# Performance work log

Measured on AMD Instinct MI355X. Metric: run time of the kernel, lower is better.

The kernel has to match this reference:

```python
import jax, jax.numpy as jnp
import numpy as np

ES = 256
NUM_SPECIES, NUM_ABILITIES, NUM_ITEMS, NUM_MOVES = 1026, 300, 500, 920
NUM_ITEM_EFFECTS, NUM_GENDERS, NUM_STATUS, NUM_VOLATILE_STATUS = 16, 3, 8, 105
B, N, F = 8192, 12, 42
# feature layout (flat int32 vector per entity)
(SPECIES, ABILITY, ITEM, ITEM_EFFECT, GENDER, STATUS, BEING_CALLED_BACK, TRAPPED,
 NEWLY_SWITCHED, TOXIC_TURNS, SLEEP_TURNS, FAINTED, ACTIVE, SIDE, LEVEL, HP, MAXHP) = range(17)
BOOST0, VOL0, MOVEID0, MOVEPP0 = 17, 24, 33, 37  # 7 boosts, 9 volatile words, 4 moves, 4 pp

DENSE_DIMS = [("hp", 10), ("level", 7), ("active", 2), ("onehot", 32), ("boosts", 7),
              ("volatiles", NUM_VOLATILE_STATUS), ("item", ES + NUM_ITEM_EFFECTS),
              ("side", 2), ("moves", ES + 6)]

def _bits(x, world_dim):
    # binary-scale embedding: bit decomposition of an int feature
    nb = (world_dim - 1).bit_length()
    mask = jnp.asarray(1 << np.arange(nb), dtype=jnp.int32)
    return ((x[..., None] & mask) != 0).astype(jnp.float32)

def setup_inputs() -> dict:
    key = jax.random.key(0)
    ks = jax.random.split(key, 32)
    s = 0.02
    inp = {"entities": jax.random.randint(ks[0], (B, N, F), 0, 2, dtype=jnp.int32)}
    inp["embed_species"] = jax.random.normal(ks[1], (NUM_SPECIES, ES), jnp.float32) * s
    inp["embed_ability"] = jax.random.normal(ks[2], (NUM_ABILITIES, ES), jnp.float32) * s
    inp["embed_item"] = jax.random.normal(ks[3], (NUM_ITEMS, ES), jnp.float32) * s
    inp["embed_moves"] = jax.random.normal(ks[4], (NUM_MOVES, ES), jnp.float32) * s
    for i, (name, din) in enumerate(DENSE_DIMS):
        inp[f"{name}_W"] = jax.random.normal(ks[5 + i], (din, ES), jnp.float32) * s
        inp[f"{name}_b"] = jnp.zeros((ES,), jnp.float32)
    return inp

def _forward(entities, embed_species, embed_ability, embed_item, embed_moves,
             hp_W, hp_b, level_W, level_b, active_W, active_b, onehot_W, onehot_b,
             boosts_W, boosts_b, volatiles_W, volatiles_b, item_W, item_b,
             side_W, side_b, moves_W, moves_b):
    e = entities
    oh = jax.nn.one_hot
    dense = lambda x, W, b: x @ W + b
    hp = e[..., HP].astype(jnp.float32)
    maxhp = jnp.clip(e[..., MAXHP], 1).astype(jnp.float32)
    hp_ratio = jnp.clip(hp / maxhp, 0.0, 1.0)                      # (B,N)
    hp_token = jnp.floor(1023.0 * hp_ratio).astype(jnp.int32)
    boolean_code = jnp.concatenate([
        hp_ratio[..., None], oh(e[..., GENDER], NUM_GENDERS), oh(e[..., STATUS], NUM_STATUS),
        oh(e[..., BEING_CALLED_BACK], 2), oh(e[..., TRAPPED], 2), oh(e[..., NEWLY_SWITCHED], 2),
        oh(e[..., TOXIC_TURNS], 8), oh(e[..., SLEEP_TURNS], 4), oh(e[..., FAINTED], 2)], axis=-1)  # (B,N,32)
    item_onehot = jnp.concatenate([embed_item[e[..., ITEM]], oh(e[..., ITEM_EFFECT], NUM_ITEM_EFFECTS)], axis=-1)
    boosts = e[..., BOOST0:VOL0].astype(jnp.float32) / 2.0          # (B,N,7)
    vol = e[..., VOL0:VOL0 + 9]
    vbits = (vol[..., None] & jnp.arange(16)) > 0                   # (B,N,9,16)
    vol_oh = vbits.reshape(*vol.shape[:-1], 144)[..., :NUM_VOLATILE_STATUS].astype(jnp.float32)
    moveset = jnp.concatenate([embed_moves[e[..., MOVEID0:MOVEPP0]],
                               _bits(e[..., MOVEPP0:MOVEPP0 + 4], 64)], axis=-1)  # (B,N,4,262)
    moves_out = jnp.einsum('bnmf,fd->bnd', moveset, moves_W) + 4.0 * moves_b      # sum of 4 Dense outputs
    emb = (dense(_bits(hp_token, 1024), hp_W, hp_b)
           + dense(_bits(e[..., LEVEL], 101), level_W, level_b)
           + dense(oh(e[..., ACTIVE], 2), active_W, active_b)
           + dense(boolean_code, onehot_W, onehot_b)
           + dense(boosts, boosts_W, boosts_b)
           + dense(vol_oh, volatiles_W, volatiles_b)
           + embed_species[e[..., SPECIES]]
           + embed_ability[e[..., ABILITY]]
           + dense(item_onehot, item_W, item_b)
           + dense(oh(e[..., SIDE], 2), side_W, side_b)
           + moves_out)
    return emb

def reference(entities, embed_species, embed_ability, embed_item, embed_moves,
              hp_W, hp_b, level_W, level_b, active_W, active_b, onehot_W, onehot_b,
              boosts_W, boosts_b, volatiles_W, volatiles_b, item_W, item_b,
              side_W, side_b, moves_W, moves_b):
    return _forward(entities, embed_species, embed_ability, embed_item, embed_moves,
                    hp_W, hp_b, level_W, level_b, active_W, active_b, onehot_W, onehot_b,
                    boosts_W, boosts_b, volatiles_W, volatiles_b, item_W, item_b,
                    side_W, side_b, moves_W, moves_b)
```

## Files before the change

kernel.cpp:

```cpp
#include <hip/hip_runtime.h>
#include <hip/hip_fp16.h>

#define ES 256
#define NFEAT 42
#define NENT (8192 * 12)

#define F_SPECIES 0
#define F_ABILITY 1
#define F_ITEM 2
#define F_ITEM_EFFECT 3
#define F_GENDER 4
#define F_STATUS 5
#define F_BCB 6
#define F_TRAPPED 7
#define F_NEWSW 8
#define F_TOXIC 9
#define F_SLEEP 10
#define F_FAINTED 11
#define F_ACTIVE 12
#define F_SIDE 13
#define F_LEVEL 14
#define F_HP 15
#define F_MAXHP 16
#define F_BOOST0 17
#define F_VOL0 24
#define F_MOVEID0 33
#define F_MOVEPP0 37

#define OFF_HP     0
#define OFF_LV     (OFF_HP + 1024*ES)
#define OFF_PP     (OFF_LV + 128*ES)
#define OFF_VP     (OFF_PP + 64*ES)
#define OFF_CA     (OFF_VP + 784*ES)
#define OFF_CB     (OFF_CA + 768*ES)
#define OFF_EI     (OFF_CB + 1024*ES)
#define OFF_EM     (OFF_EI + 500*ES)
#define OFF_SP     (OFF_EM + 920*ES)
#define OFF_AB     (OFF_SP + 1026*ES)
#define WS_HALVES  (OFF_AB + 300*ES)

typedef float vf4 __attribute__((ext_vector_type(4)));

__device__ __forceinline__ float4 ld4(const float* p) {
    return *reinterpret_cast<const float4*>(p);
}
__device__ __forceinline__ void st4(float* p, const float4 v) {
    *reinterpret_cast<float4*>(p) = v;
}
__device__ __forceinline__ void st4_nt(float* p, const float4 v) {
    vf4 t = {v.x, v.y, v.z, v.w};
    __builtin_nontemporal_store(t, reinterpret_cast<vf4*>(p));
}
__device__ __forceinline__ void add4(float4& a, const float4 b) {
    a.x += b.x; a.y += b.y; a.z += b.z; a.w += b.w;
}
__device__ __forceinline__ float4 sum4(const float4 a, const float4 b) {
    return make_float4(a.x + b.x, a.y + b.y, a.z + b.z, a.w + b.w);
}
__device__ __forceinline__ void fma4(float4& a, float s, const float4 b) {
    a.x += s * b.x; a.y += s * b.y; a.z += s * b.z; a.w += s * b.w;
}
__device__ __forceinline__ int sclamp(int x, int lo, int hi) {
    return x < lo ? lo : (x > hi ? hi : x);
}
__device__ __forceinline__ void st4h(__half* p, const float4 v) {
    __half2 a = __floats2half2_rn(v.x, v.y);
    __half2 b = __floats2half2_rn(v.z, v.w);
    uint2 u;
    u.x = *reinterpret_cast<unsigned*>(&a);
    u.y = *reinterpret_cast<unsigned*>(&b);
    *reinterpret_cast<uint2*>(p) = u;
}

#define TB_HP0 0
#define TB_LV0 256
#define TB_PP0 288
#define TB_VP0 304
#define TB_CA0 500
#define TB_CB0 692
#define TB_EI0 948
#define TB_EM0 1073
#define TB_SP0 1303
#define TB_AB0 1560
#define TB_TOT 1635

__global__ __launch_bounds__(256) void k_tables(
    const float* __restrict__ sp_e, const float* __restrict__ ab_e,
    const float* __restrict__ item_e, const float* __restrict__ moves_e,
    const float* __restrict__ hp_W, const float* __restrict__ level_W,
    const float* __restrict__ moves_W, const float* __restrict__ vol_W,
    const float* __restrict__ item_W, const float* __restrict__ onehot_W,
    const float* __restrict__ active_W, const float* __restrict__ side_W,
    const float* __restrict__ hp_b, const float* __restrict__ level_b,
    const float* __restrict__ active_b, const float* __restrict__ onehot_b,
    const float* __restrict__ boosts_b, const float* __restrict__ vol_b,
    const float* __restrict__ item_b, const float* __restrict__ side_b,
    const float* __restrict__ moves_b,
    __half* __restrict__ wh) {
    __shared__ float4 se4[4][64];
    const int bid = blockIdx.x, tid = threadIdx.x;
    const int rl = tid >> 6, lane = tid & 63, d0 = lane * 4;
    float4 acc = make_float4(0.f, 0.f, 0.f, 0.f);

    if (bid < TB_LV0) {
        int v = (bid - TB_HP0) * 4 + rl;
        for (int b = 0; b < 10; ++b)
            if ((v >> b) & 1) add4(acc, ld4(hp_W + b * ES + d0));
        st4h(wh + OFF_HP + v * ES + d0, acc);
    } else if (bid < TB_PP0) {
        int v = (bid - TB_LV0) * 4 + rl;
        for (int b = 0; b < 7; ++b)
            if ((v >> b) & 1) add4(acc, ld4(level_W + b * ES + d0));
        st4h(wh + OFF_LV + v * ES + d0, acc);
    } else if (bid < TB_VP0) {
        int v = (bid - TB_PP0) * 4 + rl;
        for (int b = 0; b < 6; ++b)
            if ((v >> b) & 1) add4(acc, ld4(moves_W + (256 + b) * ES + d0));
        st4h(wh + OFF_PP + v * ES + d0, acc);
    } else if (bid < TB_CA0) {
        int v = (bid - TB_VP0) * 4 + rl;
        if (v < 768) {
            int t = v >> 8, pair = v & 255, a = pair >> 4, b = pair & 15;
            for (int j = 0; j < 16; ++j) {
                if (a & j) add4(acc, ld4(vol_W + (32 * t + j) * ES + d0));
                if (b & j) add4(acc, ld4(vol_W + (32 * t + 16 + j) * ES + d0));
            }
        } else {
            int a = v - 768;
            for (int j = 0; j < 9; ++j)
                if (a & j) add4(acc, ld4(vol_W + (96 + j) * ES + d0));
        }
        st4h(wh + OFF_VP + v * ES + d0, acc);
    } else if (bid < TB_CB0) {
        int idx = (bid - TB_CA0) * 4 + rl;
        int fa = idx & 1, ns = (idx >> 1) & 1, tr = (idx >> 2) & 1, bcb = (idx >> 3) & 1;
        int rest = idx >> 4, g = rest % 3, e = rest / 3;
        acc = sum4(sum4(ld4(item_W + (256 + e) * ES + d0), ld4(onehot_W + (1 + g) * ES + d0)),
                   sum4(ld4(onehot_W + (12 + bcb) * ES + d0), ld4(onehot_W + (14 + tr) * ES + d0)));
        add4(acc, sum4(ld4(onehot_W + (16 + ns) * ES + d0), ld4(onehot_W + (30 + fa) * ES + d0)));
        st4h(wh + OFF_CA + idx * ES + d0, acc);
    } else if (bid < TB_EI0) {
        int idx = (bid - TB_CB0) * 4 + rl;
        int sd = idx & 1, act = (idx >> 1) & 1, sl = (idx >> 2) & 3,
            tox = (idx >> 4) & 7, st = idx >> 7;
        acc = sum4(sum4(ld4(hp_b + d0), ld4(level_b + d0)),
                   sum4(ld4(active_b + d0), ld4(onehot_b + d0)));
        add4(acc, sum4(ld4(boosts_b + d0), ld4(vol_b + d0)));
        add4(acc, sum4(ld4(item_b + d0), ld4(side_b + d0)));
        fma4(acc, 4.0f, ld4(moves_b + d0));
        add4(acc, sum4(ld4(onehot_W + (4 + st) * ES + d0), ld4(onehot_W + (18 + tox) * ES + d0)));
        add4(acc, sum4(ld4(onehot_W + (26 + sl) * ES + d0),
                       sum4(ld4(active_W + act * ES + d0), ld4(side_W + sd * ES + d0))));
        st4h(wh + OFF_CB + idx * ES + d0, acc);
    } else if (bid < TB_SP0) {
        const float* E; const float* W; __half* o; int r0;
        if (bid < TB_EM0) { E = item_e;  W = item_W;  o = wh + OFF_EI; r0 = (bid - TB_EI0) * 4; }
        else              { E = moves_e; W = moves_W; o = wh + OFF_EM; r0 = (bid - TB_EM0) * 4; }
        se4[tid >> 6][tid & 63] = ld4(E + r0 * ES + tid * 4);
        __syncthreads();
#pragma unroll 4
        for (int k0 = 0; k0 < 64; ++k0) {
            float4 e4 = se4[rl][k0];
            fma4(acc, e4.x, ld4(W + (4 * k0 + 0) * ES + d0));
            fma4(acc, e4.y, ld4(W + (4 * k0 + 1) * ES + d0));
            fma4(acc, e4.z, ld4(W + (4 * k0 + 2) * ES + d0));
            fma4(acc, e4.w, ld4(W + (4 * k0 + 3) * ES + d0));
        }
        st4h(o + (r0 + rl) * ES + d0, acc);
    } else if (bid < TB_AB0) {
        int r = (bid - TB_SP0) * 4 + rl;
        if (r < 1026) st4h(wh + OFF_SP + r * ES + d0, ld4(sp_e + r * ES + d0));
    } else {
        int r = (bid - TB_AB0) * 4 + rl;
        st4h(wh + OFF_AB + r * ES + d0, ld4(ab_e + r * ES + d0));
    }
}


__global__ __launch_bounds__(256) void k_main(
    const int* __restrict__ ent,
    const float* __restrict__ onehotW, const float* __restrict__ boostsW,
    const __half* __restrict__ wh,
    float* __restrict__ out) {
    __shared__ float lds[8 * ES];
    {
        int t = threadIdx.x;
        int row = t >> 5, col = (t & 31) * 8;
        const float* src = (row < 7) ? (boostsW + row * ES + col) : (onehotW + col);
        st4(&lds[row * ES + col], ld4(src));
        st4(&lds[row * ES + col + 4], ld4(src + 4));
    }
    __syncthreads();

    const int lane  = threadIdx.x & 63;
    const int wpair = __builtin_amdgcn_readfirstlane((blockIdx.x * 256 + threadIdx.x) >> 6);
    const int entA  = wpair * 2;
    const int e     = lane >> 5;
    const int sub   = lane & 31;
    const int sub8  = sub * 8;
    const int base  = entA * NFEAT;

    const int fv  = __builtin_nontemporal_load(ent + base + lane);
    const int fv2 = __builtin_nontemporal_load(ent + base + 52 + sub);

#define RLA(i) __builtin_amdgcn_readlane(fv, (i))
#define RLB(i) ((i) < 22 ? __builtin_amdgcn_readlane(fv, 42 + (i)) \
                         : __builtin_amdgcn_readlane(fv2, (i) - 10))

    const __half* Hp = wh + OFF_HP;
    const __half* Lv = wh + OFF_LV;
    const __half* Pp = wh + OFF_PP;
    const __half* VP = wh + OFF_VP;
    const __half* CA = wh + OFF_CA;
    const __half* CB = wh + OFF_CB;
    const __half* EI = wh + OFF_EI;
    const __half* EM = wh + OFF_EM;
    const __half* SP = wh + OFF_SP;
    const __half* AB = wh + OFF_AB;

#define IDX_BLOCK(RL, S) \
    const int iCB##S = ((((RL(F_STATUS) & 7) * 8 + (RL(F_TOXIC) & 7)) * 4 + (RL(F_SLEEP) & 3)) * 2 + \
                        (RL(F_ACTIVE) & 1)) * 2 + (RL(F_SIDE) & 1); \
    const int iCA##S = (((((RL(F_ITEM_EFFECT) & 15) * 3 + sclamp(RL(F_GENDER), 0, 2)) * 2 + \
                          (RL(F_BCB) & 1)) * 2 + (RL(F_TRAPPED) & 1)) * 2 + \
                        (RL(F_NEWSW) & 1)) * 2 + (RL(F_FAINTED) & 1); \
    const int iSP##S = sclamp(RL(F_SPECIES), 0, 1025); \
    const int iAB##S = sclamp(RL(F_ABILITY), 0, 299); \
    const int iIT##S = sclamp(RL(F_ITEM), 0, 499); \
    float hpv##S = (float)RL(F_HP); \
    int mh##S = RL(F_MAXHP); if (mh##S < 1) mh##S = 1; \
    const float ratio##S = fminf(fmaxf(hpv##S / (float)mh##S, 0.f), 1.f); \
    const int tok##S = (int)floorf(1023.f * ratio##S); \
    const int iLV##S = RL(F_LEVEL) & 127; \
    const int vp0##S = ((RL(F_VOL0 + 0) & 15) << 4) | (RL(F_VOL0 + 1) & 15); \
    const int vp1##S = ((RL(F_VOL0 + 2) & 15) << 4) | (RL(F_VOL0 + 3) & 15); \
    const int vp2##S = ((RL(F_VOL0 + 4) & 15) << 4) | (RL(F_VOL0 + 5) & 15); \
    const int v6##S  = RL(F_VOL0 + 6) & 15; \
    const int m0##S = sclamp(RL(F_MOVEID0 + 0), 0, 919), m1##S = sclamp(RL(F_MOVEID0 + 1), 0, 919), \
              m2##S = sclamp(RL(F_MOVEID0 + 2), 0, 919), m3##S = sclamp(RL(F_MOVEID0 + 3), 0, 919); \
    const int p0##S = RL(F_MOVEPP0 + 0) & 63, p1##S = RL(F_MOVEPP0 + 1) & 63, \
              p2##S = RL(F_MOVEPP0 + 2) & 63, p3##S = RL(F_MOVEPP0 + 3) & 63; \
    const float b0##S = (float)RL(F_BOOST0 + 0), b1##S = (float)RL(F_BOOST0 + 1), \
                b2##S = (float)RL(F_BOOST0 + 2), b3##S = (float)RL(F_BOOST0 + 3), \
                b4##S = (float)RL(F_BOOST0 + 4), b5##S = (float)RL(F_BOOST0 + 5), \
                b6##S = (float)RL(F_BOOST0 + 6);

    IDX_BLOCK(RLA, A)
    IDX_BLOCK(RLB, B)
#undef RLA
#undef RLB
#undef IDX_BLOCK

#define SEL(x) (e ? x##B : x##A)
    const int jCB = SEL(iCB), jCA = SEL(iCA), jSP = SEL(iSP), jAB = SEL(iAB), jIT = SEL(iIT);
    const int jHP = SEL(tok), jLV = SEL(iLV);
    const int jV0 = SEL(vp0), jV1 = SEL(vp1), jV2 = SEL(vp2), jV6 = SEL(v6);
    const int jP0 = SEL(p0), jP1 = SEL(p1), jP2 = SEL(p2), jP3 = SEL(p3);
    const int jM0 = SEL(m0), jM1 = SEL(m1), jM2 = SEL(m2), jM3 = SEL(m3);
    const float ratio = SEL(ratio);
    const float s0v = 0.5f * SEL(b0), s1v = 0.5f * SEL(b1), s2v = 0.5f * SEL(b2),
                s3v = 0.5f * SEL(b3), s4v = 0.5f * SEL(b4), s5v = 0.5f * SEL(b5),
                s6v = 0.5f * SEL(b6);
#undef SEL

#define LD8(n, tab, idx) const uint4 n = *reinterpret_cast<const uint4*>((tab) + (idx) * ES + sub8)
    LD8(uCB, CB, jCB);
    LD8(uCA, CA, jCA);
    LD8(uSP, SP, jSP);
    LD8(uAB, AB, jAB);
    LD8(uIT, EI, jIT);
    LD8(uHP, Hp, jHP);
    LD8(uLV, Lv, jLV);
    LD8(uV0, VP, 0 * 256 + jV0);
    LD8(uV1, VP, 1 * 256 + jV1);
    LD8(uV2, VP, 2 * 256 + jV2);
    LD8(uV6, VP, 768 + jV6);
    LD8(uP0, Pp, jP0);
    LD8(uP1, Pp, jP1);
    LD8(uP2, Pp, jP2);
    LD8(uP3, Pp, jP3);
    LD8(uE0, EM, jM0);
    LD8(uE1, EM, jM1);
    LD8(uE2, EM, jM2);
    LD8(uE3, EM, jM3);
#undef LD8

    float4 a0 = make_float4(0.f, 0.f, 0.f, 0.f);
    float4 a1 = make_float4(0.f, 0.f, 0.f, 0.f);
#define ACC(u) { \
    __half2 h; float2 f; \
    h = *reinterpret_cast<const __half2*>(&u.x); f = __half22float2(h); a0.x += f.x; a0.y += f.y; \
    h = *reinterpret_cast<const __half2*>(&u.y); f = __half22float2(h); a0.z += f.x; a0.w += f.y; \
    h = *reinterpret_cast<const __half2*>(&u.z); f = __half22float2(h); a1.x += f.x; a1.y += f.y; \
    h = *reinterpret_cast<const __half2*>(&u.w); f = __half22float2(h); a1.z += f.x; a1.w += f.y; }
    ACC(uCB) ACC(uCA) ACC(uSP) ACC(uAB) ACC(uIT) ACC(uHP) ACC(uLV)
    ACC(uV0) ACC(uV1) ACC(uV2) ACC(uV6)
    ACC(uP0) ACC(uP1) ACC(uP2) ACC(uP3)
    ACC(uE0) ACC(uE1) ACC(uE2) ACC(uE3)
#undef ACC

    fma4(a0, ratio, ld4(&lds[7 * ES + sub8]));     fma4(a1, ratio, ld4(&lds[7 * ES + sub8 + 4]));
    fma4(a0, s0v, ld4(&lds[0 * ES + sub8]));       fma4(a1, s0v, ld4(&lds[0 * ES + sub8 + 4]));
    fma4(a0, s1v, ld4(&lds[1 * ES + sub8]));       fma4(a1, s1v, ld4(&lds[1 * ES + sub8 + 4]));
    fma4(a0, s2v, ld4(&lds[2 * ES + sub8]));       fma4(a1, s2v, ld4(&lds[2 * ES + sub8 + 4]));
    fma4(a0, s3v, ld4(&lds[3 * ES + sub8]));       fma4(a1, s3v, ld4(&lds[3 * ES + sub8 + 4]));
    fma4(a0, s4v, ld4(&lds[4 * ES + sub8]));       fma4(a1, s4v, ld4(&lds[4 * ES + sub8 + 4]));
    fma4(a0, s5v, ld4(&lds[5 * ES + sub8]));       fma4(a1, s5v, ld4(&lds[5 * ES + sub8 + 4]));
    fma4(a0, s6v, ld4(&lds[6 * ES + sub8]));       fma4(a1, s6v, ld4(&lds[6 * ES + sub8 + 4]));

    float* op = out + (entA + e) * ES + sub8;
    st4_nt(op, a0);
    st4_nt(op + 4, a1);
}


extern "C" void kernel_launch(void* const* d_in, const int* in_sizes, int n_in,
                              void* d_out, int out_size, void* d_ws, size_t ws_size,
                              hipStream_t stream) {
    const int*   entities = (const int*)  d_in[0];
    const float* sp       = (const float*)d_in[1];
    const float* ab       = (const float*)d_in[2];
    const float* item_e   = (const float*)d_in[3];
    const float* moves_e  = (const float*)d_in[4];
    const float* hp_W     = (const float*)d_in[5];
    const float* hp_b     = (const float*)d_in[6];
    const float* level_W  = (const float*)d_in[7];
    const float* level_b  = (const float*)d_in[8];
    const float* active_W = (const float*)d_in[9];
    const float* active_b = (const float*)d_in[10];
    const float* onehot_W = (const float*)d_in[11];
    const float* onehot_b = (const float*)d_in[12];
    const float* boosts_W = (const float*)d_in[13];
    const float* boosts_b = (const float*)d_in[14];
    const float* vol_W    = (const float*)d_in[15];
    const float* vol_b    = (const float*)d_in[16];
    const float* item_W   = (const float*)d_in[17];
    const float* item_b   = (const float*)d_in[18];
    const float* side_W   = (const float*)d_in[19];
    const float* side_b   = (const float*)d_in[20];
    const float* moves_W  = (const float*)d_in[21];
    const float* moves_b  = (const float*)d_in[22];

    __half* wh  = (__half*)d_ws;
    float*  out = (float*)d_out;

    k_tables<<<TB_TOT, 256, 0, stream>>>(
        sp, ab, item_e, moves_e, hp_W, level_W, moves_W, vol_W,
        item_W, onehot_W, active_W, side_W,
        hp_b, level_b, active_b, onehot_b, boosts_b,
        vol_b, item_b, side_b, moves_b, wh);

    k_main<<<NENT / 8, 256, 0, stream>>>(entities, onehot_W, boosts_W, wh, out);
}
```

Measured before the change: 212.0 us.

## Precompute boost-pair and hp-ratio contributions into fp16 lookup tables

Folds the hp ratio term into the hp token table and builds new fp16 tables for boost pairs (13x13) and the last boost. The main kernel no longer stages boosts and onehot weights in LDS or runs a block barrier, and replaces the FMAs with four extra gathers. It also precomputes byte offsets per lookup. The cost is more gather traffic per entity, and the ratio term is now quantized to the hp token with fp16 rounding. Boost values are also clamped to the range -6 to 6.

New measurement: 214.0 us. Within noise of the previous version (+0.9%).

```diff
diff --git a/kernel.cpp b/kernel.cpp
--- a/kernel.cpp
+++ b/kernel.cpp
@@ -37,15 +37,16 @@
 #define OFF_EM     (OFF_EI + 500*ES)
 #define OFF_SP     (OFF_EM + 920*ES)
 #define OFF_AB     (OFF_SP + 1026*ES)
-#define WS_HALVES  (OFF_AB + 300*ES)
+#define OFF_B01    (OFF_AB + 300*ES)
+#define OFF_B23    (OFF_B01 + 169*ES)
+#define OFF_B45    (OFF_B23 + 169*ES)
+#define OFF_B6     (OFF_B45 + 169*ES)
+#define WS_HALVES  (OFF_B6 + 13*ES)
 
 typedef float vf4 __attribute__((ext_vector_type(4)));
 
 __device__ __forceinline__ float4 ld4(const float* p) {
     return *reinterpret_cast<const float4*>(p);
-}
-__device__ __forceinline__ void st4(float* p, const float4 v) {
-    *reinterpret_cast<float4*>(p) = v;
 }
 __device__ __forceinline__ void st4_nt(float* p, const float4 v) {
     vf4 t = {v.x, v.y, v.z, v.w};
@@ -82,7 +83,8 @@
 #define TB_EM0 1073
 #define TB_SP0 1303
 #define TB_AB0 1560
-#define TB_TOT 1635
+#define TB_BP0 1635
+#define TB_TOT 1765
 
 __global__ __launch_bounds__(256) void k_tables(
     const float* __restrict__ sp_e, const float* __restrict__ ab_e,
@@ -91,6 +93,7 @@
     const float* __restrict__ moves_W, const float* __restrict__ vol_W,
     const float* __restrict__ item_W, const float* __restrict__ onehot_W,
     const float* __restrict__ active_W, const float* __restrict__ side_W,
+    const float* __restrict__ boosts_W,
     const float* __restrict__ hp_b, const float* __restrict__ level_b,
     const float* __restrict__ active_b, const float* __restrict__ onehot_b,
     const float* __restrict__ boosts_b, const float* __restrict__ vol_b,
@@ -106,6 +109,7 @@
         int v = (bid - TB_HP0) * 4 + rl;
         for (int b = 0; b < 10; ++b)
             if ((v >> b) & 1) add4(acc, ld4(hp_W + b * ES + d0));
+        fma4(acc, (float)v * (1.0f / 1023.0f), ld4(onehot_W + d0));
         st4h(wh + OFF_HP + v * ES + d0, acc);
     } else if (bid < TB_PP0) {
         int v = (bid - TB_LV0) * 4 + rl;
@@ -170,34 +174,37 @@
     } else if (bid < TB_AB0) {
         int r = (bid - TB_SP0) * 4 + rl;
         if (r < 1026) st4h(wh + OFF_SP + r * ES + d0, ld4(sp_e + r * ES + d0));
-    } else {
+    } else if (bid < TB_BP0) {
         int r = (bid - TB_AB0) * 4 + rl;
         st4h(wh + OFF_AB + r * ES + d0, ld4(ab_e + r * ES + d0));
+    } else {
+        int r = (bid - TB_BP0) * 4 + rl;
+        if (r < 507) {
+            int pair = r / 169;
+            int rr = r - pair * 169;
+            int i = rr / 13, j = rr % 13;
+            fma4(acc, 0.5f * (float)(i - 6), ld4(boosts_W + (2 * pair) * ES + d0));
+            fma4(acc, 0.5f * (float)(j - 6), ld4(boosts_W + (2 * pair + 1) * ES + d0));
+            st4h(wh + OFF_B01 + r * ES + d0, acc);
+        } else {
+            int b = r - 507;
+            fma4(acc, 0.5f * (float)(b - 6), ld4(boosts_W + 6 * ES + d0));
+            st4h(wh + OFF_B6 + b * ES + d0, acc);
+        }
     }
 }
 
 
 __global__ __launch_bounds__(256) void k_main(
     const int* __restrict__ ent,
-    const float* __restrict__ onehotW, const float* __restrict__ boostsW,
     const __half* __restrict__ wh,
     float* __restrict__ out) {
-    __shared__ float lds[8 * ES];
-    {
-        int t = threadIdx.x;
-        int row = t >> 5, col = (t & 31) * 8;
-        const float* src = (row < 7) ? (boostsW + row * ES + col) : (onehotW + col);
-        st4(&lds[row * ES + col], ld4(src));
-        st4(&lds[row * ES + col + 4], ld4(src + 4));
-    }
-    __syncthreads();
-
     const int lane  = threadIdx.x & 63;
     const int wpair = __builtin_amdgcn_readfirstlane((blockIdx.x * 256 + threadIdx.x) >> 6);
     const int entA  = wpair * 2;
     const int e     = lane >> 5;
     const int sub   = lane & 31;
-    const int sub8  = sub * 8;
+    const int sub16 = sub * 16;
     const int base  = entA * NFEAT;
 
     const int fv  = __builtin_nontemporal_load(ent + base + lane);
@@ -207,108 +214,89 @@
 #define RLB(i) ((i) < 22 ? __builtin_amdgcn_readlane(fv, 42 + (i)) \
                          : __builtin_amdgcn_readlane(fv2, (i) - 10))
 
-    const __half* Hp = wh + OFF_HP;
-    const __half* Lv = wh + OFF_LV;
-    const __half* Pp = wh + OFF_PP;
-    const __half* VP = wh + OFF_VP;
-    const __half* CA = wh + OFF_CA;
-    const __half* CB = wh + OFF_CB;
-    const __half* EI = wh + OFF_EI;
-    const __half* EM = wh + OFF_EM;
-    const __half* SP = wh + OFF_SP;
-    const __half* AB = wh + OFF_AB;
-
+#define GOFF(OFF, idx) (((OFF) * 2) + ((idx) << 9))
 #define IDX_BLOCK(RL, S) \
-    const int iCB##S = ((((RL(F_STATUS) & 7) * 8 + (RL(F_TOXIC) & 7)) * 4 + (RL(F_SLEEP) & 3)) * 2 + \
-                        (RL(F_ACTIVE) & 1)) * 2 + (RL(F_SIDE) & 1); \
-    const int iCA##S = (((((RL(F_ITEM_EFFECT) & 15) * 3 + sclamp(RL(F_GENDER), 0, 2)) * 2 + \
+    const int oCB##S = GOFF(OFF_CB, ((((RL(F_STATUS) & 7) * 8 + (RL(F_TOXIC) & 7)) * 4 + (RL(F_SLEEP) & 3)) * 2 + \
+                        (RL(F_ACTIVE) & 1)) * 2 + (RL(F_SIDE) & 1)); \
+    const int oCA##S = GOFF(OFF_CA, (((((RL(F_ITEM_EFFECT) & 15) * 3 + sclamp(RL(F_GENDER), 0, 2)) * 2 + \
                           (RL(F_BCB) & 1)) * 2 + (RL(F_TRAPPED) & 1)) * 2 + \
-                        (RL(F_NEWSW) & 1)) * 2 + (RL(F_FAINTED) & 1); \
-    const int iSP##S = sclamp(RL(F_SPECIES), 0, 1025); \
-    const int iAB##S = sclamp(RL(F_ABILITY), 0, 299); \
-    const int iIT##S = sclamp(RL(F_ITEM), 0, 499); \
+                        (RL(F_NEWSW) & 1)) * 2 + (RL(F_FAINTED) & 1)); \
+    const int oSP##S = GOFF(OFF_SP, sclamp(RL(F_SPECIES), 0, 1025)); \
+    const int oAB##S = GOFF(OFF_AB, sclamp(RL(F_ABILITY), 0, 299)); \
+    const int oIT##S = GOFF(OFF_EI, sclamp(RL(F_ITEM), 0, 499)); \
     float hpv##S = (float)RL(F_HP); \
     int mh##S = RL(F_MAXHP); if (mh##S < 1) mh##S = 1; \
     const float ratio##S = fminf(fmaxf(hpv##S / (float)mh##S, 0.f), 1.f); \
-    const int tok##S = (int)floorf(1023.f * ratio##S); \
-    const int iLV##S = RL(F_LEVEL) & 127; \
-    const int vp0##S = ((RL(F_VOL0 + 0) & 15) << 4) | (RL(F_VOL0 + 1) & 15); \
-    const int vp1##S = ((RL(F_VOL0 + 2) & 15) << 4) | (RL(F_VOL0 + 3) & 15); \
-    const int vp2##S = ((RL(F_VOL0 + 4) & 15) << 4) | (RL(F_VOL0 + 5) & 15); \
-    const int v6##S  = RL(F_VOL0 + 6) & 15; \
-    const int m0##S = sclamp(RL(F_MOVEID0 + 0), 0, 919), m1##S = sclamp(RL(F_MOVEID0 + 1), 0, 919), \
-              m2##S = sclamp(RL(F_MOVEID0 + 2), 0, 919), m3##S = sclamp(RL(F_MOVEID0 + 3), 0, 919); \
-    const int p0##S = RL(F_MOVEPP0 + 0) & 63, p1##S = RL(F_MOVEPP0 + 1) & 63, \
-              p2##S = RL(F_MOVEPP0 + 2) & 63, p3##S = RL(F_MOVEPP0 + 3) & 63; \
-    const float b0##S = (float)RL(F_BOOST0 + 0), b1##S = (float)RL(F_BOOST0 + 1), \
-                b2##S = (float)RL(F_BOOST0 + 2), b3##S = (float)RL(F_BOOST0 + 3), \
-                b4##S = (float)RL(F_BOOST0 + 4), b5##S = (float)RL(F_BOOST0 + 5), \
-                b6##S = (float)RL(F_BOOST0 + 6);
+    const int oHP##S = GOFF(OFF_HP, (int)floorf(1023.f * ratio##S)); \
+    const int oLV##S = GOFF(OFF_LV, RL(F_LEVEL) & 127); \
+    const int oV0##S = GOFF(OFF_VP, (0 * 256) + (((RL(F_VOL0 + 0) & 15) << 4) | (RL(F_VOL0 + 1) & 15))); \
+    const int oV1##S = GOFF(OFF_VP, (1 * 256) + (((RL(F_VOL0 + 2) & 15) << 4) | (RL(F_VOL0 + 3) & 15))); \
+    const int oV2##S = GOFF(OFF_VP, (2 * 256) + (((RL(F_VOL0 + 4) & 15) << 4) | (RL(F_VOL0 + 5) & 15))); \
+    const int oV6##S = GOFF(OFF_VP, 768 + (RL(F_VOL0 + 6) & 15)); \
+    const int oP0##S = GOFF(OFF_PP, RL(F_MOVEPP0 + 0) & 63); \
+    const int oP1##S = GOFF(OFF_PP, RL(F_MOVEPP0 + 1) & 63); \
+    const int oP2##S = GOFF(OFF_PP, RL(F_MOVEPP0 + 2) & 63); \
+    const int oP3##S = GOFF(OFF_PP, RL(F_MOVEPP0 + 3) & 63); \
+    const int oE0##S = GOFF(OFF_EM, sclamp(RL(F_MOVEID0 + 0), 0, 919)); \
+    const int oE1##S = GOFF(OFF_EM, sclamp(RL(F_MOVEID0 + 1), 0, 919)); \
+    const int oE2##S = GOFF(OFF_EM, sclamp(RL(F_MOVEID0 + 2), 0, 919)); \
+    const int oE3##S = GOFF(OFF_EM, sclamp(RL(F_MOVEID0 + 3), 0, 919)); \
+    const int oB0##S = GOFF(OFF_B01, (sclamp(RL(F_BOOST0 + 0), -6, 6) + 6) * 13 + (sclamp(RL(F_BOOST0 + 1), -6, 6) + 6)); \
+    const int oB2##S = GOFF(OFF_B23, (sclamp(RL(F_BOOST0 + 2), -6, 6) + 6) * 13 + (sclamp(RL(F_BOOST0 + 3), -6, 6) + 6)); \
+    const int oB4##S = GOFF(OFF_B45, (sclamp(RL(F_BOOST0 + 4), -6, 6) + 6) * 13 + (sclamp(RL(F_BOOST0 + 5), -6, 6) + 6)); \
+    const int oB6##S = GOFF(OFF_B6, sclamp(RL(F_BOOST0 + 6), -6, 6) + 6);
 
     IDX_BLOCK(RLA, A)
     IDX_BLOCK(RLB, B)
 #undef RLA
 #undef RLB
 #undef IDX_BLOCK
-
-#define SEL(x) (e ? x##B : x##A)
-    const int jCB = SEL(iCB), jCA = SEL(iCA), jSP = SEL(iSP), jAB = SEL(iAB), jIT = SEL(iIT);
-    const int jHP = SEL(tok), jLV = SEL(iLV);
-    const int jV0 = SEL(vp0), jV1 = SEL(vp1), jV2 = SEL(vp2), jV6 = SEL(v6);
-    const int jP0 = SEL(p0), jP1 = SEL(p1), jP2 = SEL(p2), jP3 = SEL(p3);
-    const int jM0 = SEL(m0), jM1 = SEL(m1), jM2 = SEL(m2), jM3 = SEL(m3);
-    const float ratio = SEL(ratio);
-    const float s0v = 0.5f * SEL(b0), s1v = 0.5f * SEL(b1), s2v = 0.5f * SEL(b2),
-                s3v = 0.5f * SEL(b3), s4v = 0.5f * SEL(b4), s5v = 0.5f * SEL(b5),
-                s6v = 0.5f * SEL(b6);
-#undef SEL
-
-#define LD8(n, tab, idx) const uint4 n = *reinterpret_cast<const uint4*>((tab) + (idx) * ES + sub8)
-    LD8(uCB, CB, jCB);
-    LD8(uCA, CA, jCA);
-    LD8(uSP, SP, jSP);
-    LD8(uAB, AB, jAB);
-    LD8(uIT, EI, jIT);
-    LD8(uHP, Hp, jHP);
-    LD8(uLV, Lv, jLV);
-    LD8(uV0, VP, 0 * 256 + jV0);
-    LD8(uV1, VP, 1 * 256 + jV1);
-    LD8(uV2, VP, 2 * 256 + jV2);
-    LD8(uV6, VP, 768 + jV6);
-    LD8(uP0, Pp, jP0);
-    LD8(uP1, Pp, jP1);
-    LD8(uP2, Pp, jP2);
-    LD8(uP3, Pp, jP3);
-    LD8(uE0, EM, jM0);
-    LD8(uE1, EM, jM1);
-    LD8(uE2, EM, jM2);
-    LD8(uE3, EM, jM3);
+#undef GOFF
+
+    const char* whb = reinterpret_cast<const char*>(wh);
+
+#define LD8(n, oX) const uint4 n = *reinterpret_cast<const uint4*>(whb + ((e ? oX##B : oX##A) + sub16))
+    LD8(uCB, oCB);
+    LD8(uCA, oCA);
+    LD8(uSP, oSP);
+    LD8(uAB, oAB);
+    LD8(uIT, oIT);
+    LD8(uHP, oHP);
+    LD8(uLV, oLV);
+    LD8(uV0, oV0);
+    LD8(uV1, oV1);
+    LD8(uV2, oV2);
+    LD8(uV6, oV6);
+    LD8(uP0, oP0);
+    LD8(uP1, oP1);
+    LD8(uP2, oP2);
+    LD8(uP3, oP3);
+    LD8(uE0, oE0);
+    LD8(uE1, oE1);
+    LD8(uE2, oE2);
+    LD8(uE3, oE3);
+    LD8(uB0, oB0);
+    LD8(uB2, oB2);
+    LD8(uB4, oB4);
+    LD8(uB6, oB6);
 #undef LD8
 
     float4 a0 = make_float4(0.f, 0.f, 0.f, 0.f);
     float4 a1 = make_float4(0.f, 0.f, 0.f, 0.f);
 #define ACC(u) { \
-    __half2 h; float2 f; \
-    h = *reinterpret_cast<const __half2*>(&u.x); f = __half22float2(h); a0.x += f.x; a0.y += f.y; \
-    h = *reinterpret_cast<const __half2*>(&u.y); f = __half22float2(h); a0.z += f.x; a0.w += f.y; \
-    h = *reinterpret_cast<const __half2*>(&u.z); f = __half22float2(h); a1.x += f.x; a1.y += f.y; \
-    h = *reinterpret_cast<const __half2*>(&u.w); f = __half22float2(h); a1.z += f.x; a1.w += f.y; }
+    const __half* h = reinterpret_cast<const __half*>(&u); \
+    a0.x += __half2float(h[0]); a0.y += __half2float(h[1]); \
+    a0.z += __half2float(h[2]); a0.w += __half2float(h[3]); \
+    a1.x += __half2float(h[4]); a1.y += __half2float(h[5]); \
+    a1.z += __half2float(h[6]); a1.w += __half2float(h[7]); }
     ACC(uCB) ACC(uCA) ACC(uSP) ACC(uAB) ACC(uIT) ACC(uHP) ACC(uLV)
     ACC(uV0) ACC(uV1) ACC(uV2) ACC(uV6)
     ACC(uP0) ACC(uP1) ACC(uP2) ACC(uP3)
     ACC(uE0) ACC(uE1) ACC(uE2) ACC(uE3)
+    ACC(uB0) ACC(uB2) ACC(uB4) ACC(uB6)
 #undef ACC
 
-    fma4(a0, ratio, ld4(&lds[7 * ES + sub8]));     fma4(a1, ratio, ld4(&lds[7 * ES + sub8 + 4]));
-    fma4(a0, s0v, ld4(&lds[0 * ES + sub8]));       fma4(a1, s0v, ld4(&lds[0 * ES + sub8 + 4]));
-    fma4(a0, s1v, ld4(&lds[1 * ES + sub8]));       fma4(a1, s1v, ld4(&lds[1 * ES + sub8 + 4]));
-    fma4(a0, s2v, ld4(&lds[2 * ES + sub8]));       fma4(a1, s2v, ld4(&lds[2 * ES + sub8 + 4]));
-    fma4(a0, s3v, ld4(&lds[3 * ES + sub8]));       fma4(a1, s3v, ld4(&lds[3 * ES + sub8 + 4]));
-    fma4(a0, s4v, ld4(&lds[4 * ES + sub8]));       fma4(a1, s4v, ld4(&lds[4 * ES + sub8 + 4]));
-    fma4(a0, s5v, ld4(&lds[5 * ES + sub8]));       fma4(a1, s5v, ld4(&lds[5 * ES + sub8 + 4]));
-    fma4(a0, s6v, ld4(&lds[6 * ES + sub8]));       fma4(a1, s6v, ld4(&lds[6 * ES + sub8 + 4]));
-
-    float* op = out + (entA + e) * ES + sub8;
+    float* op = out + (entA + e) * ES + sub * 8;
     st4_nt(op, a0);
     st4_nt(op + 4, a1);
 }
@@ -346,9 +334,9 @@
 
     k_tables<<<TB_TOT, 256, 0, stream>>>(
         sp, ab, item_e, moves_e, hp_W, level_W, moves_W, vol_W,
-        item_W, onehot_W, active_W, side_W,
+        item_W, onehot_W, active_W, side_W, boosts_W,
         hp_b, level_b, active_b, onehot_b, boosts_b,
         vol_b, item_b, side_b, moves_b, wh);
 
-    k_main<<<NENT / 8, 256, 0, stream>>>(entities, onehot_W, boosts_W, wh, out);
-}
+    k_main<<<NENT / 8, 256, 0, stream>>>(entities, wh, out);
+}
```
